# Kernel optimization log

Hardware: AMD Instinct MI355X
Metric: run time of the kernel (lower is better)

The kernel has to match this reference:

```python
import jax, jax.numpy as jnp
import numpy as np

NUM_GT = 25      # num_gt_lesions (init kwarg); labels 1..25 all present in gt
NUM_PRED = 40    # number of predicted CC labels (labels 0..40 in pred)
SMOOTH = 1.0
VOL = (256, 256, 256)


def setup_inputs() -> dict:
    key = jax.random.key(0)
    k1, k2 = jax.random.split(key)
    # pred holds integer-valued connected-component labels stored as float
    # (the original applies sigmoid to it and compares values for identity).
    pred = jax.random.randint(k1, VOL, 0, NUM_PRED + 1).astype(jnp.float32)
    gt = jax.random.randint(k2, VOL, 0, NUM_GT + 1).astype(jnp.int32)
    return {"pred": pred, "gt": gt}


def _instance_dice(pred, gt):
    # Original: s = sigmoid(pred); all unique/isin/!=0 tests are on s.
    # sigmoid is injective => value equality on s == label equality on pred;
    # sigmoid(x) != 0 always  => every `!= 0` filter in the original is a no-op
    # (in particular pred label 0 participates, since sigmoid(0)=0.5).
    lbl = jax.lax.stop_gradient(jnp.round(pred)).astype(jnp.int32)  # pred CC ids
    g = gt.astype(jnp.int32)

    # Joint histogram counts[p, c] = #voxels with pred==p and gt==c.
    combined = (lbl * (NUM_GT + 1) + g).ravel()
    counts = jnp.zeros((NUM_PRED + 1) * (NUM_GT + 1), jnp.float32)
    counts = counts.at[combined].add(1.0).reshape(NUM_PRED + 1, NUM_GT + 1)

    gt_sizes = counts[:, 1:].sum(axis=0)            # [L] |gt == c| for c=1..L
    present = gt_sizes > 0
    num_gt = present.sum()                          # torch.unique(gt[gt!=0]).size(0)

    overlap = counts[:, 1:] > 0                     # [P+1, L] pred label p hits comp c
    pred_sizes = counts.sum(axis=1)                 # [P+1] |pred == p|
    union_size = (overlap * pred_sizes[:, None]).sum(axis=0)  # |pred_tmp| per comp
    # pred_tmp covers every voxel of the gt component => intersection = gt_sizes
    dice = 2.0 * gt_sizes / (union_size + gt_sizes + SMOOTH)
    lesion_dice = jnp.where(present, dice, 0.0).sum()

    tp_any = (overlap & present[None, :]).any(axis=1)  # pred labels collected in tp
    fp = ((pred_sizes > 0) & ~tp_any).sum()            # pred labels missing all gt comps
    return lesion_dice / (num_gt + fp)


def reference(pred, gt):
    return _instance_dice(pred, gt)
```

## Files before the change

kernel.cpp:

```cpp
#include <hip/hip_runtime.h>
#include <hip/hip_bf16.h>

#define NUM_GT 25
#define NUM_PRED 40
#define PAD 32

#define GT_W(b)  ((b) * PAD)
#define PR_W(p)  ((25 + (p)) * PAD)
#define OV_W(p)  ((65 + (p)) * PAD)
#define WS_WORDS (106 * PAD)

#define GRID 1024
#define BLOCK 256

__global__ __launch_bounds__(BLOCK, 4) void hist_kernel(
    const float* __restrict__ pred, const int* __restrict__ gt,
    unsigned int* __restrict__ ws, int n)
{
    __shared__ unsigned int sovl[64];
    __shared__ unsigned int shist[65];
    __shared__ unsigned int stash[4][16][34];

    const int tid  = threadIdx.x;
    const int lane = tid & 63;
    const int wave = tid >> 6;

    if (tid < 64) sovl[tid] = 0u;
    if (tid < 65) shist[tid] = 0u;
    __syncthreads();

    unsigned acc[66];
    #pragma unroll
    for (int j = 0; j < 66; ++j) acc[j] = 0u;

    const int gtid   = blockIdx.x * BLOCK + tid;
    const int stride = GRID * BLOCK;
    const int n4 = n >> 2;
    const float4* __restrict__ p4 = (const float4*)pred;
    const int4* __restrict__  g4 = (const int4*)gt;

    for (int i = gtid; i < n4; i += stride) {
        float4 pv = p4[i];
        int4  gv = g4[i];
        unsigned p0 = (unsigned)pv.x, p1 = (unsigned)pv.y;
        unsigned p2 = (unsigned)pv.z, p3 = (unsigned)pv.w;
        unsigned g0 = (unsigned)gv.x, g1 = (unsigned)gv.y;
        unsigned g2 = (unsigned)gv.z, g3 = (unsigned)gv.w;

        unsigned m0 = 1u << (g0 & 31), m1 = 1u << (g1 & 31);
        unsigned m2 = 1u << (g2 & 31), m3 = 1u << (g3 & 31);
        if (!(sovl[p0 & 63] & m0)) atomicOr(&sovl[p0 & 63], m0);
        if (!(sovl[p1 & 63] & m1)) atomicOr(&sovl[p1 & 63], m1);
        if (!(sovl[p2 & 63] & m2)) atomicOr(&sovl[p2 & 63], m2);
        if (!(sovl[p3 & 63] & m3)) atomicOr(&sovl[p3 & 63], m3);

        unsigned G4w = g0 | (g1 << 8) | (g2 << 16) | (g3 << 24);
        unsigned P4w = p0 | (p1 << 8) | (p2 << 16) | (p3 << 24);

        #pragma unroll
        for (int b = 0; b < 25; ++b)
            asm("v_sad_u8 %0, %1, %2, %0"
                : "+v"(acc[b]) : "v"(G4w), "s"((unsigned)(b * 0x01010101u)));
        #pragma unroll
        for (int b = 0; b < 40; ++b)
            asm("v_sad_u8 %0, %1, %2, %0"
                : "+v"(acc[25 + b]) : "v"(P4w), "s"((unsigned)(b * 0x01010101u)));
    }

    if (blockIdx.x == 0 && tid == 0) {
        for (int v = n4 << 2; v < n; ++v) {
            int p = (int)pred[v];
            int g = gt[v];
            for (int b = 0; b < 25; ++b) atomicAdd(&ws[GT_W(b)], (unsigned)abs(g - b));
            for (int b = 0; b < 40; ++b) atomicAdd(&ws[PR_W(b)], (unsigned)abs(p - b));
            atomicOr(&ws[OV_W(min(max(p, 0), NUM_PRED))], 1u << (g & 31));
        }
    }

    #pragma unroll
    for (int jp = 0; jp < 33; ++jp) {
        unsigned v = acc[2 * jp] | (acc[2 * jp + 1] << 16);
        v += __shfl_down(v, 32, 64);
        v += __shfl_down(v, 16, 64);
        if (lane < 16) stash[wave][lane][jp] = v;
    }
    __syncthreads();

    for (int i = tid; i < 33 * 16; i += BLOCK) {
        int jp = i >> 4, sl = i & 15;
        unsigned a = stash[0][sl][jp] + stash[1][sl][jp]
                   + stash[2][sl][jp] + stash[3][sl][jp];
        unsigned lo = a & 0xFFFFu, hi = a >> 16;
        lo += __shfl_down(lo, 8, 16);  hi += __shfl_down(hi, 8, 16);
        lo += __shfl_down(lo, 4, 16);  hi += __shfl_down(hi, 4, 16);
        lo += __shfl_down(lo, 2, 16);  hi += __shfl_down(hi, 2, 16);
        lo += __shfl_down(lo, 1, 16);  hi += __shfl_down(hi, 1, 16);
        if (sl == 0) {
            if (lo) atomicAdd(&shist[2 * jp], lo);
            if (hi && 2 * jp + 1 < 65) atomicAdd(&shist[2 * jp + 1], hi);
        }
    }
    __syncthreads();

    for (int i = tid; i < 65; i += BLOCK) {
        unsigned s = shist[i];
        if (s) atomicAdd(&ws[i * PAD], s);
    }
    if (tid < 41) {
        unsigned v = sovl[tid];
        if (v) atomicOr(&ws[OV_W(tid)], v);
    }
}

__global__ __launch_bounds__(64) void finish_kernel(
    const unsigned int* __restrict__ ws, float* __restrict__ out, int n)
{
    __shared__ long long gg[25], gp[40], psz[41];
    __shared__ unsigned ov[41];
    const int lane = threadIdx.x;
    if (lane < 25) gg[lane] = (long long)ws[GT_W(lane)];
    if (lane < 40) gp[lane] = (long long)ws[PR_W(lane)];
    if (lane < 41) ov[lane] = ws[OV_W(lane)];
    __syncthreads();

    const long long N = n, Sg = gg[0], Sp = gp[0];

    if (lane < 41) {
        int P = lane;
        long long f;
        if (P == 0)       f = (N - gp[0] + gp[1]) / 2;
        else if (P <= 38) f = (gp[P - 1] - 2 * gp[P] + gp[P + 1]) / 2;
        else if (P == 39) f = (gp[38] - 2 * gp[39] + (40 * N - Sp)) / 2;
        else              f = (gp[39] - 39 * N + Sp) / 2;
        psz[P] = f;
    }
    __syncthreads();

    double dice = 0.0;
    int present = 0;
    if (lane < 25) {
        int L = lane + 1;
        long long gs;
        if (L <= 23)      gs = (gg[L - 1] - 2 * gg[L] + gg[L + 1]) / 2;
        else if (L == 24) gs = (gg[23] - 2 * gg[24] + (25 * N - Sg)) / 2;
        else              gs = (gg[24] - 24 * N + Sg) / 2;
        if (gs > 0) {
            present = 1;
            double un = 0.0;
            const unsigned bit = 1u << L;
            for (int p = 0; p < 41; ++p)
                if (ov[p] & bit) un += (double)psz[p];
            dice = 2.0 * (double)gs / (un + (double)gs + 1.0);
        }
    }
    int fp = 0;
    if (lane < 41) {
        if (psz[lane] > 0 && (ov[lane] & 0x3FFFFFEu) == 0) fp = 1;
    }

    int num_gt = __popcll(__ballot(present != 0));
    int nfp    = __popcll(__ballot(fp != 0));
    #pragma unroll
    for (int o = 32; o >= 1; o >>= 1) dice += __shfl_xor(dice, o, 64);

    if (lane == 0) out[0] = (float)(dice / (double)(num_gt + nfp));
}

extern "C" void kernel_launch(void* const* d_in, const int* in_sizes, int n_in,
                              void* d_out, int out_size, void* d_ws, size_t ws_size,
                              hipStream_t stream) {
    const float* pred = (const float*)d_in[0];
    const int* gt = (const int*)d_in[1];
    float* out = (float*)d_out;
    unsigned int* ws = (unsigned int*)d_ws;
    const int n = in_sizes[0];

    hipMemsetAsync(ws, 0, WS_WORDS * sizeof(unsigned int), stream);

    hist_kernel<<<GRID, BLOCK, 0, stream>>>(pred, gt, ws, n);
    finish_kernel<<<1, 64, 0, stream>>>(ws, out, n);
}
```

Baseline: 47.68 us.

## Software-pipeline histogram loads, process 8 voxels per iteration, batch overlap-bit checks

The main loop now has each thread handle two adjacent float4/int4 pairs per iteration and prefetches the next iteration's data into registers before processing the current one. This is meant to hide global load latency behind the SAD arithmetic. The eight per-voxel shared-memory overlap test-and-or branches are replaced by a single combined check that only issues atomics when some bit is missing. It also adds a remainder loop, more live registers and less coalesced per-thread access, since each thread reads two consecutive float4s.

```diff
diff --git a/kernel.cpp b/kernel.cpp
--- a/kernel.cpp
+++ b/kernel.cpp
@@ -33,38 +33,99 @@
     #pragma unroll
     for (int j = 0; j < 66; ++j) acc[j] = 0u;
 
-    const int gtid   = blockIdx.x * BLOCK + tid;
-    const int stride = GRID * BLOCK;
-    const int n4 = n >> 2;
+    const int gtid = blockIdx.x * BLOCK + tid;
+    const int n4   = n >> 2;
+    const int step = GRID * BLOCK * 2;
+    const int nit  = n4 / step;
+
     const float4* __restrict__ p4 = (const float4*)pred;
     const int4* __restrict__  g4 = (const int4*)gt;
 
-    for (int i = gtid; i < n4; i += stride) {
-        float4 pv = p4[i];
-        int4  gv = g4[i];
-        unsigned p0 = (unsigned)pv.x, p1 = (unsigned)pv.y;
-        unsigned p2 = (unsigned)pv.z, p3 = (unsigned)pv.w;
-        unsigned g0 = (unsigned)gv.x, g1 = (unsigned)gv.y;
-        unsigned g2 = (unsigned)gv.z, g3 = (unsigned)gv.w;
-
-        unsigned m0 = 1u << (g0 & 31), m1 = 1u << (g1 & 31);
-        unsigned m2 = 1u << (g2 & 31), m3 = 1u << (g3 & 31);
-        if (!(sovl[p0 & 63] & m0)) atomicOr(&sovl[p0 & 63], m0);
-        if (!(sovl[p1 & 63] & m1)) atomicOr(&sovl[p1 & 63], m1);
-        if (!(sovl[p2 & 63] & m2)) atomicOr(&sovl[p2 & 63], m2);
-        if (!(sovl[p3 & 63] & m3)) atomicOr(&sovl[p3 & 63], m3);
-
-        unsigned G4w = g0 | (g1 << 8) | (g2 << 16) | (g3 << 24);
-        unsigned P4w = p0 | (p1 << 8) | (p2 << 16) | (p3 << 24);
-
+    #define PROC8(PV0, PV1, GV0, GV1)                                          \
+    do {                                                                       \
+        unsigned a0 = (unsigned)(GV0).x, a1 = (unsigned)(GV0).y;               \
+        unsigned a2 = (unsigned)(GV0).z, a3 = (unsigned)(GV0).w;               \
+        unsigned a4 = (unsigned)(GV1).x, a5 = (unsigned)(GV1).y;               \
+        unsigned a6 = (unsigned)(GV1).z, a7 = (unsigned)(GV1).w;               \
+        unsigned b0 = (unsigned)(PV0).x, b1 = (unsigned)(PV0).y;               \
+        unsigned b2 = (unsigned)(PV0).z, b3 = (unsigned)(PV0).w;               \
+        unsigned b4 = (unsigned)(PV1).x, b5 = (unsigned)(PV1).y;               \
+        unsigned b6 = (unsigned)(PV1).z, b7 = (unsigned)(PV1).w;               \
+        unsigned ok = (sovl[b0 & 63] >> (a0 & 31)) & (sovl[b1 & 63] >> (a1 & 31)) \
+                    & (sovl[b2 & 63] >> (a2 & 31)) & (sovl[b3 & 63] >> (a3 & 31)) \
+                    & (sovl[b4 & 63] >> (a4 & 31)) & (sovl[b5 & 63] >> (a5 & 31)) \
+                    & (sovl[b6 & 63] >> (a6 & 31)) & (sovl[b7 & 63] >> (a7 & 31)); \
+        if (!(ok & 1u)) {                                                      \
+            atomicOr(&sovl[b0 & 63], 1u << (a0 & 31));                         \
+            atomicOr(&sovl[b1 & 63], 1u << (a1 & 31));                         \
+            atomicOr(&sovl[b2 & 63], 1u << (a2 & 31));                         \
+            atomicOr(&sovl[b3 & 63], 1u << (a3 & 31));                         \
+            atomicOr(&sovl[b4 & 63], 1u << (a4 & 31));                         \
+            atomicOr(&sovl[b5 & 63], 1u << (a5 & 31));                         \
+            atomicOr(&sovl[b6 & 63], 1u << (a6 & 31));                         \
+            atomicOr(&sovl[b7 & 63], 1u << (a7 & 31));                         \
+        }                                                                      \
+        unsigned GA = a0 | (a1 << 8) | (a2 << 16) | (a3 << 24);                \
+        unsigned GB = a4 | (a5 << 8) | (a6 << 16) | (a7 << 24);                \
+        unsigned PA = b0 | (b1 << 8) | (b2 << 16) | (b3 << 24);                \
+        unsigned PB = b4 | (b5 << 8) | (b6 << 16) | (b7 << 24);                \
+        _Pragma("unroll")                                                      \
+        for (int b = 0; b < 25; ++b) {                                         \
+            asm("v_sad_u8 %0, %1, %2, %0"                                      \
+                : "+v"(acc[b]) : "v"(GA), "s"((unsigned)(b * 0x01010101u)));   \
+            asm("v_sad_u8 %0, %1, %2, %0"                                      \
+                : "+v"(acc[b]) : "v"(GB), "s"((unsigned)(b * 0x01010101u)));   \
+        }                                                                      \
+        _Pragma("unroll")                                                      \
+        for (int b = 0; b < 40; ++b) {                                         \
+            asm("v_sad_u8 %0, %1, %2, %0"                                      \
+                : "+v"(acc[25+b]) : "v"(PA), "s"((unsigned)(b * 0x01010101u)));\
+            asm("v_sad_u8 %0, %1, %2, %0"                                      \
+                : "+v"(acc[25+b]) : "v"(PB), "s"((unsigned)(b * 0x01010101u)));\
+        }                                                                      \
+    } while (0)
+
+    if (nit > 0) {
+        int q = gtid * 2;
+        float4 pA0 = p4[q], pA1 = p4[q + 1];
+        int4  gA0 = g4[q], gA1 = g4[q + 1];
+        for (int it = 0; it < nit; ++it) {
+            const int qn = (it + 1 < nit) ? (q + step) : q;
+            float4 pB0 = p4[qn], pB1 = p4[qn + 1];
+            int4  gB0 = g4[qn], gB1 = g4[qn + 1];
+
+            PROC8(pA0, pA1, gA0, gA1);
+
+            pA0 = pB0; pA1 = pB1; gA0 = gB0; gA1 = gB1;
+            q += step;
+        }
+    }
+
+    for (int qq = nit * step + gtid; qq < n4; qq += GRID * BLOCK) {
+        float4 pv = p4[qq];
+        int4  gv = g4[qq];
+        unsigned a0 = (unsigned)gv.x, a1 = (unsigned)gv.y;
+        unsigned a2 = (unsigned)gv.z, a3 = (unsigned)gv.w;
+        unsigned b0 = (unsigned)pv.x, b1 = (unsigned)pv.y;
+        unsigned b2 = (unsigned)pv.z, b3 = (unsigned)pv.w;
+        unsigned ok = (sovl[b0 & 63] >> (a0 & 31)) & (sovl[b1 & 63] >> (a1 & 31))
+                    & (sovl[b2 & 63] >> (a2 & 31)) & (sovl[b3 & 63] >> (a3 & 31));
+        if (!(ok & 1u)) {
+            atomicOr(&sovl[b0 & 63], 1u << (a0 & 31));
+            atomicOr(&sovl[b1 & 63], 1u << (a1 & 31));
+            atomicOr(&sovl[b2 & 63], 1u << (a2 & 31));
+            atomicOr(&sovl[b3 & 63], 1u << (a3 & 31));
+        }
+        unsigned GA = a0 | (a1 << 8) | (a2 << 16) | (a3 << 24);
+        unsigned PA = b0 | (b1 << 8) | (b2 << 16) | (b3 << 24);
         #pragma unroll
         for (int b = 0; b < 25; ++b)
             asm("v_sad_u8 %0, %1, %2, %0"
-                : "+v"(acc[b]) : "v"(G4w), "s"((unsigned)(b * 0x01010101u)));
+                : "+v"(acc[b]) : "v"(GA), "s"((unsigned)(b * 0x01010101u)));
         #pragma unroll
         for (int b = 0; b < 40; ++b)
             asm("v_sad_u8 %0, %1, %2, %0"
-                : "+v"(acc[25 + b]) : "v"(P4w), "s"((unsigned)(b * 0x01010101u)));
+                : "+v"(acc[25+b]) : "v"(PA), "s"((unsigned)(b * 0x01010101u)));
     }
 
     if (blockIdx.x == 0 && tid == 0) {
@@ -110,6 +171,7 @@
         unsigned v = sovl[tid];
         if (v) atomicOr(&ws[OV_W(tid)], v);
     }
+    #undef PROC8
 }
 
 __global__ __launch_bounds__(64) void finish_kernel(
```

Measured after the change: 48.04 us. About the same (+0.8%).

## Stage packed tiles in LDS and split SAD histogram bins across waves

Applied to the files above, without the earlier changes.

The histogram kernel now loads 8192-voxel tiles, packs the byte labels into LDS, and has each wave run v_sad_u8 over the whole tile for its own subset of bins. Each thread no longer carries 65 accumulators across the entire grid-stride loop, and the multi-stage stash reduction is replaced by per-bin wave reductions. Global atomics are spread over 64 rows that the finish kernel sums, which reduces contention. The overlap bitmask check is also batched so that all four voxels are tested in a single branch. The cost is two block barriers per tile, extra LDS traffic, and uneven work across waves (17, 16, 16 and 16 bins).

```diff
diff --git a/kernel.cpp b/kernel.cpp
--- a/kernel.cpp
+++ b/kernel.cpp
@@ -3,23 +3,56 @@
 
 #define NUM_GT 25
 #define NUM_PRED 40
-#define PAD 32
-
-#define GT_W(b)  ((b) * PAD)
-#define PR_W(p)  ((25 + (p)) * PAD)
-#define OV_W(p)  ((65 + (p)) * PAD)
-#define WS_WORDS (106 * PAD)
-
-#define GRID 1024
+#define TILE 8192
+#define TILE_W (TILE / 4)
+#define GRID 2048
 #define BLOCK 256
 
-__global__ __launch_bounds__(BLOCK, 4) void hist_kernel(
+#define WS_OV    4160
+#define WS_WORDS (4160 + 41)
+
+template <int NB>
+__device__ __forceinline__ void sad_scan_flush(
+    const unsigned* __restrict__ src, int kbase, int sbin0,
+    unsigned* shist, int lane)
+{
+    unsigned acc[NB];
+    #pragma unroll
+    for (int b = 0; b < NB; ++b) acc[b] = 0u;
+
+    #pragma unroll
+    for (int j = 0; j < TILE_W / (64 * 4); ++j) {
+        const uint4 w = *(const uint4*)&src[(lane + j * 64) * 4];
+        #pragma unroll
+        for (int b = 0; b < NB; ++b) {
+            const unsigned K = (unsigned)((kbase + b) * 0x01010101u);
+            asm("v_sad_u8 %0, %1, %2, %0" : "+v"(acc[b]) : "v"(w.x), "s"(K));
+            asm("v_sad_u8 %0, %1, %2, %0" : "+v"(acc[b]) : "v"(w.y), "s"(K));
+            asm("v_sad_u8 %0, %1, %2, %0" : "+v"(acc[b]) : "v"(w.z), "s"(K));
+            asm("v_sad_u8 %0, %1, %2, %0" : "+v"(acc[b]) : "v"(w.w), "s"(K));
+        }
+    }
+    #pragma unroll
+    for (int b = 0; b < NB; ++b) {
+        unsigned c = acc[b];
+        c += __shfl_down(c, 32, 64);
+        c += __shfl_down(c, 16, 64);
+        c += __shfl_down(c, 8, 64);
+        c += __shfl_down(c, 4, 64);
+        c += __shfl_down(c, 2, 64);
+        c += __shfl_down(c, 1, 64);
+        if (lane == 0) atomicAdd(&shist[sbin0 + b], c);
+    }
+}
+
+__global__ __launch_bounds__(BLOCK) void hist_kernel(
     const float* __restrict__ pred, const int* __restrict__ gt,
-    unsigned int* __restrict__ ws, int n)
+    unsigned* __restrict__ ws, int n)
 {
-    __shared__ unsigned int sovl[64];
-    __shared__ unsigned int shist[65];
-    __shared__ unsigned int stash[4][16][34];
+    __shared__ __align__(16) unsigned lds_gt[TILE_W];
+    __shared__ __align__(16) unsigned lds_pr[TILE_W];
+    __shared__ unsigned sovl[64];
+    __shared__ unsigned shist[65];
 
     const int tid  = threadIdx.x;
     const int lane = tid & 63;
@@ -29,141 +62,134 @@
     if (tid < 65) shist[tid] = 0u;
     __syncthreads();
 
-    unsigned acc[66];
-    #pragma unroll
-    for (int j = 0; j < 66; ++j) acc[j] = 0u;
-
-    const int gtid   = blockIdx.x * BLOCK + tid;
-    const int stride = GRID * BLOCK;
-    const int n4 = n >> 2;
+    const int ntiles = n / TILE;
     const float4* __restrict__ p4 = (const float4*)pred;
     const int4* __restrict__  g4 = (const int4*)gt;
 
-    for (int i = gtid; i < n4; i += stride) {
-        float4 pv = p4[i];
-        int4  gv = g4[i];
-        unsigned p0 = (unsigned)pv.x, p1 = (unsigned)pv.y;
-        unsigned p2 = (unsigned)pv.z, p3 = (unsigned)pv.w;
-        unsigned g0 = (unsigned)gv.x, g1 = (unsigned)gv.y;
-        unsigned g2 = (unsigned)gv.z, g3 = (unsigned)gv.w;
-
-        unsigned m0 = 1u << (g0 & 31), m1 = 1u << (g1 & 31);
-        unsigned m2 = 1u << (g2 & 31), m3 = 1u << (g3 & 31);
-        if (!(sovl[p0 & 63] & m0)) atomicOr(&sovl[p0 & 63], m0);
-        if (!(sovl[p1 & 63] & m1)) atomicOr(&sovl[p1 & 63], m1);
-        if (!(sovl[p2 & 63] & m2)) atomicOr(&sovl[p2 & 63], m2);
-        if (!(sovl[p3 & 63] & m3)) atomicOr(&sovl[p3 & 63], m3);
-
-        unsigned G4w = g0 | (g1 << 8) | (g2 << 16) | (g3 << 24);
-        unsigned P4w = p0 | (p1 << 8) | (p2 << 16) | (p3 << 24);
+    for (int tile = blockIdx.x; tile < ntiles; tile += GRID) {
+        const int wbase = tile * TILE_W;
 
         #pragma unroll
-        for (int b = 0; b < 25; ++b)
-            asm("v_sad_u8 %0, %1, %2, %0"
-                : "+v"(acc[b]) : "v"(G4w), "s"((unsigned)(b * 0x01010101u)));
-        #pragma unroll
-        for (int b = 0; b < 40; ++b)
-            asm("v_sad_u8 %0, %1, %2, %0"
-                : "+v"(acc[25 + b]) : "v"(P4w), "s"((unsigned)(b * 0x01010101u)));
+        for (int it = 0; it < TILE_W / BLOCK; ++it) {
+            const int w = it * BLOCK + tid;
+            int4  g = g4[wbase + w];
+            float4 p = p4[wbase + w];
+            unsigned a0=(unsigned)g.x, a1=(unsigned)g.y;
+            unsigned a2=(unsigned)g.z, a3=(unsigned)g.w;
+            unsigned b0=(unsigned)p.x, b1=(unsigned)p.y;
+            unsigned b2=(unsigned)p.z, b3=(unsigned)p.w;
+
+            unsigned ok = (sovl[b0 & 63] >> (a0 & 31))
+                        & (sovl[b1 & 63] >> (a1 & 31))
+                        & (sovl[b2 & 63] >> (a2 & 31))
+                        & (sovl[b3 & 63] >> (a3 & 31));
+            if (!(ok & 1u)) {
+                atomicOr(&sovl[b0 & 63], 1u << (a0 & 31));
+                atomicOr(&sovl[b1 & 63], 1u << (a1 & 31));
+                atomicOr(&sovl[b2 & 63], 1u << (a2 & 31));
+                atomicOr(&sovl[b3 & 63], 1u << (a3 & 31));
+            }
+            lds_gt[w] = a0 | (a1 << 8) | (a2 << 16) | (a3 << 24);
+            lds_pr[w] = b0 | (b1 << 8) | (b2 << 16) | (b3 << 24);
+        }
+        __syncthreads();
+
+        if (wave == 0) {
+            sad_scan_flush<17>(lds_gt, 0, 0, shist, lane);
+        } else if (wave == 1) {
+            sad_scan_flush<8>(lds_gt, 17, 17, shist, lane);
+            sad_scan_flush<8>(lds_pr, 0, 25, shist, lane);
+        } else if (wave == 2) {
+            sad_scan_flush<16>(lds_pr, 8, 33, shist, lane);
+        } else {
+            sad_scan_flush<16>(lds_pr, 24, 49, shist, lane);
+        }
+        __syncthreads();
     }
 
     if (blockIdx.x == 0 && tid == 0) {
-        for (int v = n4 << 2; v < n; ++v) {
+        for (int v = ntiles * TILE; v < n; ++v) {
             int p = (int)pred[v];
             int g = gt[v];
-            for (int b = 0; b < 25; ++b) atomicAdd(&ws[GT_W(b)], (unsigned)abs(g - b));
-            for (int b = 0; b < 40; ++b) atomicAdd(&ws[PR_W(b)], (unsigned)abs(p - b));
-            atomicOr(&ws[OV_W(min(max(p, 0), NUM_PRED))], 1u << (g & 31));
-        }
-    }
-
-    #pragma unroll
-    for (int jp = 0; jp < 33; ++jp) {
-        unsigned v = acc[2 * jp] | (acc[2 * jp + 1] << 16);
-        v += __shfl_down(v, 32, 64);
-        v += __shfl_down(v, 16, 64);
-        if (lane < 16) stash[wave][lane][jp] = v;
-    }
-    __syncthreads();
-
-    for (int i = tid; i < 33 * 16; i += BLOCK) {
-        int jp = i >> 4, sl = i & 15;
-        unsigned a = stash[0][sl][jp] + stash[1][sl][jp]
-                   + stash[2][sl][jp] + stash[3][sl][jp];
-        unsigned lo = a & 0xFFFFu, hi = a >> 16;
-        lo += __shfl_down(lo, 8, 16);  hi += __shfl_down(hi, 8, 16);
-        lo += __shfl_down(lo, 4, 16);  hi += __shfl_down(hi, 4, 16);
-        lo += __shfl_down(lo, 2, 16);  hi += __shfl_down(hi, 2, 16);
-        lo += __shfl_down(lo, 1, 16);  hi += __shfl_down(hi, 1, 16);
-        if (sl == 0) {
-            if (lo) atomicAdd(&shist[2 * jp], lo);
-            if (hi && 2 * jp + 1 < 65) atomicAdd(&shist[2 * jp + 1], hi);
-        }
-    }
-    __syncthreads();
-
-    for (int i = tid; i < 65; i += BLOCK) {
-        unsigned s = shist[i];
-        if (s) atomicAdd(&ws[i * PAD], s);
+            for (int b = 0; b < 25; ++b) atomicAdd(&ws[b], (unsigned)abs(g - b));
+            for (int b = 0; b < 40; ++b) atomicAdd(&ws[25 + b], (unsigned)abs(p - b));
+            atomicOr(&ws[WS_OV + min(max(p, 0), NUM_PRED)], 1u << (g & 31));
+        }
+    }
+
+    __syncthreads();
+    const int row = blockIdx.x & 63;
+    if (tid < 65) {
+        unsigned s = shist[tid];
+        if (s) atomicAdd(&ws[row * 65 + tid], s);
     }
     if (tid < 41) {
         unsigned v = sovl[tid];
-        if (v) atomicOr(&ws[OV_W(tid)], v);
-    }
-}
-
-__global__ __launch_bounds__(64) void finish_kernel(
-    const unsigned int* __restrict__ ws, float* __restrict__ out, int n)
+        if (v) atomicOr(&ws[WS_OV + tid], v);
+    }
+}
+
+__global__ __launch_bounds__(128) void finish_kernel(
+    const unsigned* __restrict__ ws, float* __restrict__ out, int n)
 {
-    __shared__ long long gg[25], gp[40], psz[41];
-    __shared__ unsigned ov[41];
-    const int lane = threadIdx.x;
-    if (lane < 25) gg[lane] = (long long)ws[GT_W(lane)];
-    if (lane < 40) gp[lane] = (long long)ws[PR_W(lane)];
-    if (lane < 41) ov[lane] = ws[OV_W(lane)];
-    __syncthreads();
-
-    const long long N = n, Sg = gg[0], Sp = gp[0];
-
-    if (lane < 41) {
-        int P = lane;
+    __shared__ long long gsum[65];
+    __shared__ long long psz[41];
+    __shared__ unsigned ovs[41];
+    const int t = threadIdx.x;
+
+    if (t < 65) {
+        unsigned s = 0;
+        for (int r = 0; r < 64; ++r) s += ws[r * 65 + t];
+        gsum[t] = (long long)s;
+    }
+    if (t < 41) ovs[t] = ws[WS_OV + t];
+    __syncthreads();
+
+    const long long N = n;
+    if (t < 41) {
+        const long long Sp = gsum[25];
+        int P = t;
         long long f;
-        if (P == 0)       f = (N - gp[0] + gp[1]) / 2;
-        else if (P <= 38) f = (gp[P - 1] - 2 * gp[P] + gp[P + 1]) / 2;
-        else if (P == 39) f = (gp[38] - 2 * gp[39] + (40 * N - Sp)) / 2;
-        else              f = (gp[39] - 39 * N + Sp) / 2;
+        if (P == 0)       f = (N - gsum[25 + 0] + gsum[25 + 1]) / 2;
+        else if (P <= 38) f = (gsum[25 + P - 1] - 2 * gsum[25 + P] + gsum[25 + P + 1]) / 2;
+        else if (P == 39) f = (gsum[25 + 38] - 2 * gsum[25 + 39] + (40 * N - Sp)) / 2;
+        else              f = (gsum[25 + 39] - 39 * N + Sp) / 2;
         psz[P] = f;
     }
     __syncthreads();
 
-    double dice = 0.0;
-    int present = 0;
-    if (lane < 25) {
-        int L = lane + 1;
-        long long gs;
-        if (L <= 23)      gs = (gg[L - 1] - 2 * gg[L] + gg[L + 1]) / 2;
-        else if (L == 24) gs = (gg[23] - 2 * gg[24] + (25 * N - Sg)) / 2;
-        else              gs = (gg[24] - 24 * N + Sg) / 2;
-        if (gs > 0) {
-            present = 1;
-            double un = 0.0;
-            const unsigned bit = 1u << L;
-            for (int p = 0; p < 41; ++p)
-                if (ov[p] & bit) un += (double)psz[p];
-            dice = 2.0 * (double)gs / (un + (double)gs + 1.0);
-        }
-    }
-    int fp = 0;
-    if (lane < 41) {
-        if (psz[lane] > 0 && (ov[lane] & 0x3FFFFFEu) == 0) fp = 1;
-    }
-
-    int num_gt = __popcll(__ballot(present != 0));
-    int nfp    = __popcll(__ballot(fp != 0));
-    #pragma unroll
-    for (int o = 32; o >= 1; o >>= 1) dice += __shfl_xor(dice, o, 64);
-
-    if (lane == 0) out[0] = (float)(dice / (double)(num_gt + nfp));
+    if (t < 64) {
+        const int lane = t;
+        const long long Sg = gsum[0];
+        double dice = 0.0;
+        int present = 0;
+        if (lane < 25) {
+            int L = lane + 1;
+            long long gs;
+            if (L <= 23)      gs = (gsum[L - 1] - 2 * gsum[L] + gsum[L + 1]) / 2;
+            else if (L == 24) gs = (gsum[23] - 2 * gsum[24] + (25 * N - Sg)) / 2;
+            else              gs = (gsum[24] - 24 * N + Sg) / 2;
+            if (gs > 0) {
+                present = 1;
+                double un = 0.0;
+                const unsigned bit = 1u << L;
+                for (int p = 0; p < 41; ++p)
+                    if (ovs[p] & bit) un += (double)psz[p];
+                dice = 2.0 * (double)gs / (un + (double)gs + 1.0);
+            }
+        }
+        int fp = 0;
+        if (lane < 41) {
+            if (psz[lane] > 0 && (ovs[lane] & 0x3FFFFFEu) == 0) fp = 1;
+        }
+
+        int num_gt = __popcll(__ballot(present != 0));
+        int nfp    = __popcll(__ballot(fp != 0));
+        #pragma unroll
+        for (int o = 32; o >= 1; o >>= 1) dice += __shfl_xor(dice, o, 64);
+
+        if (lane == 0) out[0] = (float)(dice / (double)(num_gt + nfp));
+    }
 }
 
 extern "C" void kernel_launch(void* const* d_in, const int* in_sizes, int n_in,
@@ -172,11 +198,11 @@
     const float* pred = (const float*)d_in[0];
     const int* gt = (const int*)d_in[1];
     float* out = (float*)d_out;
-    unsigned int* ws = (unsigned int*)d_ws;
+    unsigned* ws = (unsigned*)d_ws;
     const int n = in_sizes[0];
 
-    hipMemsetAsync(ws, 0, WS_WORDS * sizeof(unsigned int), stream);
+    hipMemsetAsync(ws, 0, WS_WORDS * sizeof(unsigned), stream);
 
     hist_kernel<<<GRID, BLOCK, 0, stream>>>(pred, gt, ws, n);
-    finish_kernel<<<1, 64, 0, stream>>>(ws, out, n);
-}
+    finish_kernel<<<1, 128, 0, stream>>>(ws, out, n);
+}
```

New measurement: 69.25 us. +45.2%, slower.
